# Kernel optimization log

Hardware: AMD Instinct MI355X
Metric: run time of the kernel (lower is better)

Reference implementation:

```python
import jax, jax.numpy as jnp
import numpy as np

SEQ = 32768
D_ENC = 200   # hardcoded input dim of nn.Linear(200, hidden_size)
H = 8192      # hidden_size


def setup_inputs() -> dict:
    key = jax.random.key(0)
    k1, k2, k3, k4 = jax.random.split(key, 4)
    hidden = jax.random.normal(k1, (H,), dtype=jnp.float32)
    encoder_outputs = jax.random.normal(k2, (SEQ, D_ENC), dtype=jnp.float32)
    # nn.Linear(200, H): weight [H, 200], bias [H]; scaled like torch default init
    bound = 1.0 / np.sqrt(D_ENC)
    W = jax.random.uniform(k3, (H, D_ENC), dtype=jnp.float32, minval=-bound, maxval=bound)
    b = jax.random.uniform(k4, (H,), dtype=jnp.float32, minval=-bound, maxval=bound)
    return {"hidden": hidden, "encoder_outputs": encoder_outputs, "W": W, "b": b}


def reference(hidden, encoder_outputs, W, b):
    # 'general' scoring: energy_i = hidden . (W @ enc_i + b), batched over all i.
    # einsum contracts without materializing the [SEQ, H] projection.
    energies = jnp.einsum('sd,hd,h->s', encoder_outputs, W, hidden) + jnp.dot(b, hidden)
    # F.softmax over the 1-D energies, then unsqueeze twice -> [1, 1, SEQ]
    attn = jax.nn.softmax(energies)
    return attn[None, None, :]
```

## Files before the change

### kernel.cpp

```cpp
#include <hip/hip_runtime.h>
#include <math.h>

#define SEQ   32768
#define DENC  200
#define NH    8192

#define K1B       128
#define K1T       512
#define K1ROWS_PB (NH / K1B)
#define K1ROWS_PG (K1ROWS_PB / 2)

#define K2B    512
#define K2T    512
#define K2ROWS (SEQ / K2B)
#define RPW    8

#define K3B    (SEQ / 256)


__device__ __forceinline__ double wave_sum_d(double x) {
    #pragma unroll
    for (int off = 32; off; off >>= 1) x += __shfl_xor(x, off, 64);
    return x;
}
__device__ __forceinline__ float wave_sum(float x) {
    #pragma unroll
    for (int off = 32; off; off >>= 1) x += __shfl_xor(x, off, 64);
    return x;
}

__global__ __launch_bounds__(K1T) void k1_proj(const float* __restrict__ W,
                                               const float* __restrict__ hidden,
                                               float* __restrict__ ws_v) {
    __shared__ float part[2][DENC];
    const int t = threadIdx.x, b = blockIdx.x;
    const int g = t >> 8, lt = t & 255;
    const int h0 = b * K1ROWS_PB + g * K1ROWS_PG;

    if (lt < DENC) {
        float acc = 0.f;
        #pragma unroll 8
        for (int i = 0; i < K1ROWS_PG; ++i)
            acc = fmaf(W[(size_t)(h0 + i) * DENC + lt], hidden[h0 + i], acc);
        part[g][lt] = acc;
    }
    __syncthreads();
    if (t < DENC)
        ws_v[b * DENC + t] = part[0][t] + part[1][t];
}

__global__ __launch_bounds__(K2T) void k2_energy(const float* __restrict__ enc,
                                                 const float* __restrict__ ws_v,
                                                 double* __restrict__ ws_p,
                                                 double* __restrict__ ws_sum) {
    __shared__ float  v_lds[DENC];
    __shared__ double s_lds[K2T / 64];
    const int t = threadIdx.x, b = blockIdx.x;
    const int lane = t & 63, wid = t >> 6;
    const bool act = (lane < 50);

    const int s0 = b * K2ROWS + wid * RPW;
    const float* ebase = enc + (size_t)s0 * DENC + lane * 4;
    float4 q0 = *(const float4*)(act ? ebase + 0*DENC : enc);
    float4 q1 = *(const float4*)(act ? ebase + 1*DENC : enc);
    float4 q2 = *(const float4*)(act ? ebase + 2*DENC : enc);
    float4 q3 = *(const float4*)(act ? ebase + 3*DENC : enc);
    float4 q4 = *(const float4*)(act ? ebase + 4*DENC : enc);
    float4 q5 = *(const float4*)(act ? ebase + 5*DENC : enc);
    float4 q6 = *(const float4*)(act ? ebase + 6*DENC : enc);
    float4 q7 = *(const float4*)(act ? ebase + 7*DENC : enc);

    if (t < DENC) {
        float a0 = 0.f, a1 = 0.f, a2 = 0.f, a3 = 0.f;
        const float* p = ws_v + t;
        #pragma unroll 4
        for (int k = 0; k < K1B; k += 4) {
            a0 += p[(size_t)(k + 0) * DENC];
            a1 += p[(size_t)(k + 1) * DENC];
            a2 += p[(size_t)(k + 2) * DENC];
            a3 += p[(size_t)(k + 3) * DENC];
        }
        v_lds[t] = (a0 + a1) + (a2 + a3);
    }
    __syncthreads();

    float4 v4 = make_float4(0.f, 0.f, 0.f, 0.f);
    if (act) v4 = *(const float4*)(v_lds + lane * 4);

    float e0,e1,e2,e3,e4,e5,e6,e7;
    #define DOT(qi, ei) { \
        float d = act ? (qi.x*v4.x + qi.y*v4.y + qi.z*v4.z + qi.w*v4.w) : 0.f; \
        ei = wave_sum(d); }
    DOT(q0,e0) DOT(q1,e1) DOT(q2,e2) DOT(q3,e3)
    DOT(q4,e4) DOT(q5,e5) DOT(q6,e6) DOT(q7,e7)
    #undef DOT

    float e = e0;
    e = (lane == 1) ? e1 : e;  e = (lane == 2) ? e2 : e;
    e = (lane == 3) ? e3 : e;  e = (lane == 4) ? e4 : e;
    e = (lane == 5) ? e5 : e;  e = (lane == 6) ? e6 : e;
    e = (lane == 7) ? e7 : e;
    double ps = 0.0;
    if (lane < 8) {
        const float f = e * 1.4426950408889634f;
        const float n = rintf(f);
        const float m = exp2f(f - n);
        const long long eb = ((long long)(1023 + (int)n)) << 52;
        ps = (double)m * __longlong_as_double(eb);
        ws_p[s0 + lane] = ps;
    }
    double p = ps;
    p += __shfl_xor(p, 1, 64);
    p += __shfl_xor(p, 2, 64);
    p += __shfl_xor(p, 4, 64);
    if (lane == 0) s_lds[wid] = p;
    __syncthreads();
    if (t == 0) {
        double S = 0.0;
        #pragma unroll
        for (int w = 0; w < K2T / 64; ++w) S += s_lds[w];
        ws_sum[b] = S;
    }
}

__global__ __launch_bounds__(256) void k3_norm(const double* __restrict__ ws_p,
                                               const double* __restrict__ ws_sum,
                                               float* __restrict__ out) {
    __shared__ double s_lds[4];
    __shared__ double inv_lds;
    const int t = threadIdx.x, b = blockIdx.x;
    const int lane = t & 63, wid = t >> 6;

    double a = ws_sum[t] + ws_sum[t + 256];
    a = wave_sum_d(a);
    if (lane == 0) s_lds[wid] = a;
    __syncthreads();
    if (t == 0) inv_lds = 1.0 / ((s_lds[0] + s_lds[1]) + (s_lds[2] + s_lds[3]));
    __syncthreads();

    const int i = b * 256 + t;
    out[i] = (float)(ws_p[i] * inv_lds);
}

extern "C" void kernel_launch(void* const* d_in, const int* in_sizes, int n_in,
                              void* d_out, int out_size, void* d_ws, size_t ws_size,
                              hipStream_t stream) {
    const float* hidden = (const float*)d_in[0];
    const float* enc    = (const float*)d_in[1];
    const float* W      = (const float*)d_in[2];
    float* out = (float*)d_out;

    float*  ws_v   = (float*)d_ws;
    double* ws_p   = (double*)(ws_v + K1B * DENC);
    double* ws_sum = ws_p + SEQ;

    k1_proj  <<<K1B, K1T, 0, stream>>>(W, hidden, ws_v);
    k2_energy<<<K2B, K2T, 0, stream>>>(enc, ws_v, ws_p, ws_sum);
    k3_norm  <<<K3B, 256, 0, stream>>>(ws_p, ws_sum, out);
}
```

Measured before the change: 20.43 us.

## Split partial-v reduction into a separate kernel and transpose partial layout

The W^T·hidden projection now runs on 256 blocks with a single row group each and writes partial sums transposed as [DENC][K1B]. A new small kernel reduces each column's 256 partials with one wave and float4 loads. Every k2 block then loads the finished vector instead of each of its 512 blocks redundantly summing 128 partials. This adds a fourth kernel launch and the extra launch latency that comes with it.

```diff
diff --git a/kernel.cpp b/kernel.cpp
--- a/kernel.cpp
+++ b/kernel.cpp
@@ -5,10 +5,9 @@
 #define DENC  200
 #define NH    8192
 
-#define K1B       128
-#define K1T       512
-#define K1ROWS_PB (NH / K1B)
-#define K1ROWS_PG (K1ROWS_PB / 2)
+#define K1B    256
+#define K1T    256
+#define K1ROWS (NH / K1B)
 
 #define K2B    512
 #define K2T    512
@@ -32,25 +31,28 @@
 __global__ __launch_bounds__(K1T) void k1_proj(const float* __restrict__ W,
                                                const float* __restrict__ hidden,
                                                float* __restrict__ ws_v) {
-    __shared__ float part[2][DENC];
     const int t = threadIdx.x, b = blockIdx.x;
-    const int g = t >> 8, lt = t & 255;
-    const int h0 = b * K1ROWS_PB + g * K1ROWS_PG;
-
-    if (lt < DENC) {
+    const int h0 = b * K1ROWS;
+    if (t < DENC) {
         float acc = 0.f;
         #pragma unroll 8
-        for (int i = 0; i < K1ROWS_PG; ++i)
-            acc = fmaf(W[(size_t)(h0 + i) * DENC + lt], hidden[h0 + i], acc);
-        part[g][lt] = acc;
+        for (int i = 0; i < K1ROWS; ++i)
+            acc = fmaf(W[(size_t)(h0 + i) * DENC + t], hidden[h0 + i], acc);
+        ws_v[(size_t)t * K1B + b] = acc;
     }
-    __syncthreads();
-    if (t < DENC)
-        ws_v[b * DENC + t] = part[0][t] + part[1][t];
+}
+
+__global__ __launch_bounds__(64) void k15_reduce(const float* __restrict__ ws_v,
+                                                 float* __restrict__ vfin) {
+    const int d = blockIdx.x, l = threadIdx.x;
+    const float4 f = *(const float4*)(ws_v + (size_t)d * K1B + 4 * l);
+    float a = (f.x + f.y) + (f.z + f.w);
+    a = wave_sum(a);
+    if (l == 0) vfin[d] = a;
 }
 
 __global__ __launch_bounds__(K2T) void k2_energy(const float* __restrict__ enc,
-                                                 const float* __restrict__ ws_v,
+                                                 const float* __restrict__ vfin,
                                                  double* __restrict__ ws_p,
                                                  double* __restrict__ ws_sum) {
     __shared__ float  v_lds[DENC];
@@ -70,18 +72,7 @@
     float4 q6 = *(const float4*)(act ? ebase + 6*DENC : enc);
     float4 q7 = *(const float4*)(act ? ebase + 7*DENC : enc);
 
-    if (t < DENC) {
-        float a0 = 0.f, a1 = 0.f, a2 = 0.f, a3 = 0.f;
-        const float* p = ws_v + t;
-        #pragma unroll 4
-        for (int k = 0; k < K1B; k += 4) {
-            a0 += p[(size_t)(k + 0) * DENC];
-            a1 += p[(size_t)(k + 1) * DENC];
-            a2 += p[(size_t)(k + 2) * DENC];
-            a3 += p[(size_t)(k + 3) * DENC];
-        }
-        v_lds[t] = (a0 + a1) + (a2 + a3);
-    }
+    if (t < DENC) v_lds[t] = vfin[t];
     __syncthreads();
 
     float4 v4 = make_float4(0.f, 0.f, 0.f, 0.f);
@@ -151,10 +142,12 @@
     float* out = (float*)d_out;
 
     float*  ws_v   = (float*)d_ws;
-    double* ws_p   = (double*)(ws_v + K1B * DENC);
+    float*  vfin   = ws_v + (size_t)DENC * K1B;
+    double* ws_p   = (double*)(vfin + DENC + 56);
     double* ws_sum = ws_p + SEQ;
 
-    k1_proj  <<<K1B, K1T, 0, stream>>>(W, hidden, ws_v);
-    k2_energy<<<K2B, K2T, 0, stream>>>(enc, ws_v, ws_p, ws_sum);
-    k3_norm  <<<K3B, 256, 0, stream>>>(ws_p, ws_sum, out);
+    k1_proj   <<<K1B,  K1T, 0, stream>>>(W, hidden, ws_v);
+    k15_reduce<<<DENC, 64,  0, stream>>>(ws_v, vfin);
+    k2_energy <<<K2B,  K2T, 0, stream>>>(enc, vfin, ws_p, ws_sum);
+    k3_norm   <<<K3B,  256, 0, stream>>>(ws_p, ws_sum, out);
 }
```

Measured after the change: 19.79 us. -3.2%, faster.
